# Kernel optimization log

Hardware: AMD Instinct MI355X
Metric: run time of the kernel (lower is better)

The kernel has to match this reference:

```python
import jax, jax.numpy as jnp
import numpy as np
from jax import lax

H = 20  # hidden_size


def _rnn_layer(x_seq, h0, W_ih, W_hh, b_ih, b_hh):
    """Vanilla tanh RNN layer. x_seq: [B,T,D], h0: [B,H]. Returns ([B,T,H], [B,H])."""
    # Precompute input projection for all timesteps (the only large GEMM).
    xp = jnp.einsum('btd,hd->bth', x_seq, W_ih) + b_ih + b_hh  # [B,T,H]

    def step(h, xt):
        h = jnp.tanh(xt + h @ W_hh.T)
        return h, h

    h_last, hs = lax.scan(step, h0, jnp.swapaxes(xp, 0, 1))  # hs: [T,B,H]
    return jnp.swapaxes(hs, 0, 1), h_last


def setup_inputs() -> dict:
    key = jax.random.key(0)
    ks = jax.random.split(key, 12)
    B, T = 4096, 512
    s = 1.0 / np.sqrt(H)  # PyTorch default uniform(-1/sqrt(H), 1/sqrt(H))
    u = lambda k, shape: jax.random.uniform(k, shape, jnp.float32, -s, s)
    return {
        'x': jax.random.normal(ks[0], (B, T, 1), jnp.float32),
        'hidden': jax.random.normal(ks[1], (2, B, H), jnp.float32),
        'W_ih0': u(ks[2], (H, 1)),
        'W_hh0': u(ks[3], (H, H)),
        'b_ih0': u(ks[4], (H,)),
        'b_hh0': u(ks[5], (H,)),
        'W_ih1': u(ks[6], (H, H)),
        'W_hh1': u(ks[7], (H, H)),
        'b_ih1': u(ks[8], (H,)),
        'b_hh1': u(ks[9], (H,)),
        'fc_w': u(ks[10], (1, H)),
        'fc_b': u(ks[11], (1,)),
    }


def reference(x, hidden, W_ih0, W_hh0, b_ih0, b_hh0, W_ih1, W_hh1, b_ih1, b_hh1, fc_w, fc_b):
    # 2-layer vanilla RNN (eval mode: inter-layer dropout disabled)
    h0_seq, h0_last = _rnn_layer(x, hidden[0], W_ih0, W_hh0, b_ih0, b_hh0)
    h1_seq, h1_last = _rnn_layer(h0_seq, hidden[1], W_ih1, W_hh1, b_ih1, b_hh1)
    out = h1_seq[:, -1, :] @ fc_w.T + fc_b  # [B,1]
    new_hidden = jnp.stack([h0_last, h1_last], axis=0)  # [2,B,H]
    return out, new_hidden
```

## Files before the change

### kernel.cpp

```cpp
#include <hip/hip_runtime.h>


#define Bsz 4096
#define Tn  512
#define Hn  20
#define GB  2
#define XPAD 520
#define NTHREADS 64

typedef float v2 __attribute__((ext_vector_type(2)));

__device__ __forceinline__ float tanh_fast(float v) {
    float e = __expf(2.0f * v);
    return 1.0f - 2.0f * __builtin_amdgcn_rcpf(e + 1.0f);
}

#define DOT20P(acc, accb, W, H) do { \
    acc  = __builtin_elementwise_fma(W##0, H##0, acc);  \
    accb = __builtin_elementwise_fma(W##1, H##1, accb); \
    acc  = __builtin_elementwise_fma(W##2, H##2, acc);  \
    accb = __builtin_elementwise_fma(W##3, H##3, accb); \
    acc  = __builtin_elementwise_fma(W##4, H##4, acc);  \
    accb = __builtin_elementwise_fma(W##5, H##5, accb); \
    acc  = __builtin_elementwise_fma(W##6, H##6, acc);  \
    accb = __builtin_elementwise_fma(W##7, H##7, accb); \
    acc  = __builtin_elementwise_fma(W##8, H##8, acc);  \
    accb = __builtin_elementwise_fma(W##9, H##9, accb); \
} while (0)

#define LOAD_ROWP(W, ptr) \
    v2 W##0, W##1, W##2, W##3, W##4, W##5, W##6, W##7, W##8, W##9; \
    { const float4* _p = (const float4*)(ptr); \
      float4 _t; \
      _t = _p[0]; W##0 = (v2){_t.x, _t.y}; W##1 = (v2){_t.z, _t.w}; \
      _t = _p[1]; W##2 = (v2){_t.x, _t.y}; W##3 = (v2){_t.z, _t.w}; \
      _t = _p[2]; W##4 = (v2){_t.x, _t.y}; W##5 = (v2){_t.z, _t.w}; \
      _t = _p[3]; W##6 = (v2){_t.x, _t.y}; W##7 = (v2){_t.z, _t.w}; \
      _t = _p[4]; W##8 = (v2){_t.x, _t.y}; W##9 = (v2){_t.z, _t.w}; }

#define READ_H(H, base) \
    v2 H##0, H##1, H##2, H##3, H##4, H##5, H##6, H##7, H##8, H##9; \
    { const float4 _a = *(const float4*)((base) + 0);  \
      const float4 _b = *(const float4*)((base) + 4);  \
      const float4 _c = *(const float4*)((base) + 8);  \
      const float4 _d = *(const float4*)((base) + 12); \
      const float4 _e = *(const float4*)((base) + 16); \
      H##0 = (v2){_a.x, _a.y}; H##1 = (v2){_a.z, _a.w}; \
      H##2 = (v2){_b.x, _b.y}; H##3 = (v2){_b.z, _b.w}; \
      H##4 = (v2){_c.x, _c.y}; H##5 = (v2){_c.z, _c.w}; \
      H##6 = (v2){_d.x, _d.y}; H##7 = (v2){_d.z, _d.w}; \
      H##8 = (v2){_e.x, _e.y}; H##9 = (v2){_e.z, _e.w}; }

__global__ __launch_bounds__(NTHREADS)
__attribute__((amdgpu_waves_per_eu(1, 2)))
void rnn2_fused(const float* __restrict__ x,
                const float* __restrict__ hidden,
                const float* __restrict__ W_ih0,
                const float* __restrict__ W_hh0,
                const float* __restrict__ b_ih0,
                const float* __restrict__ b_hh0,
                const float* __restrict__ W_ih1,
                const float* __restrict__ W_hh1,
                const float* __restrict__ b_ih1,
                const float* __restrict__ b_hh1,
                const float* __restrict__ fc_w,
                const float* __restrict__ fc_b,
                float* __restrict__ out)
{
    const int tid = threadIdx.x;
    int g = tid / Hn;
    int j = tid - g * Hn;
    if (g >= GB) { g = GB - 1; j = tid % Hn; }
    const int  b        = blockIdx.x * GB + g;
    const bool b_ok     = (b < Bsz);
    const int  bl       = b_ok ? b : (Bsz - 1);
    const bool store_ok = (tid < GB * Hn) && b_ok;

    __shared__ float xs[GB][XPAD];
    __shared__ float hs[2][GB][Hn];

    LOAD_ROWP(w0, W_hh0 + j * Hn)
    LOAD_ROWP(w1, W_ih1 + j * Hn)
    LOAD_ROWP(w2, W_hh1 + j * Hn)

    const float wih0  = W_ih0[j];
    const float bias0 = b_ih0[j] + b_hh0[j];
    const float bias1 = b_ih1[j] + b_hh1[j];

    {
        const int bB = blockIdx.x * GB;
        #pragma unroll
        for (int r = 0; r < (GB * Tn) / (NTHREADS * 4); ++r) {
            const int c  = (r * NTHREADS + tid) * 4;
            const int gg = c >> 9;
            const int t  = c & (Tn - 1);
            const int bb = (bB + gg < Bsz) ? (bB + gg) : (Bsz - 1);
            float4 v = *(const float4*)(x + (long)bb * Tn + t);
            *(float4*)&xs[gg][t] = v;
        }
    }

    hs[0][g][j] = hidden[bl * Hn + j];
    hs[1][g][j] = hidden[(long)Bsz * Hn + bl * Hn + j];

    {
        READ_H(hA, &hs[0][g][0])
        v2 a0  = (v2){fmaf(xs[g][0], wih0, bias0), 0.f};
        v2 a0b = (v2){0.f, 0.f};
        DOT20P(a0, a0b, w0, hA);
        v2 s0 = a0 + a0b;
        hs[0][g][j] = tanh_fast(s0.x + s0.y);
    }

    #pragma unroll 4
    for (int i = 1; i < Tn; ++i) {
        READ_H(hA, &hs[0][g][0])
        READ_H(hB, &hs[1][g][0])

        const float xt = xs[g][i];

        v2 a0  = (v2){fmaf(xt, wih0, bias0), 0.f};
        v2 a0b = (v2){0.f, 0.f};
        v2 a1  = (v2){bias1, 0.f};
        v2 a1b = (v2){0.f, 0.f};
        v2 a2  = (v2){0.f, 0.f};
        v2 a2b = (v2){0.f, 0.f};
        DOT20P(a0, a0b, w0, hA);
        DOT20P(a1, a1b, w1, hA);
        DOT20P(a2, a2b, w2, hB);

        const v2 s0 = a0 + a0b;
        const v2 s1 = (a1 + a1b) + (a2 + a2b);
        const float n0 = tanh_fast(s0.x + s0.y);
        const float n1 = tanh_fast(s1.x + s1.y);
        hs[0][g][j] = n0;
        hs[1][g][j] = n1;
    }

    {
        READ_H(hA, &hs[0][g][0])
        READ_H(hB, &hs[1][g][0])
        v2 a1  = (v2){bias1, 0.f};
        v2 a1b = (v2){0.f, 0.f};
        v2 a2  = (v2){0.f, 0.f};
        v2 a2b = (v2){0.f, 0.f};
        DOT20P(a1, a1b, w1, hA);
        DOT20P(a2, a2b, w2, hB);
        const v2 s1 = (a1 + a1b) + (a2 + a2b);
        hs[1][g][j] = tanh_fast(s1.x + s1.y);
    }

    if (store_ok) {
        out[Bsz + (long)b * Hn + j]                  = hs[0][g][j];
        out[Bsz + (long)Bsz * Hn + (long)b * Hn + j] = hs[1][g][j];
        if (j == 0) {
            LOAD_ROWP(fw, fc_w)
            READ_H(hv, &hs[1][g][0])
            v2 aA = (v2){fc_b[0], 0.f};
            v2 aB = (v2){0.f, 0.f};
            DOT20P(aA, aB, fw, hv);
            const v2 s = aA + aB;
            out[b] = s.x + s.y;
        }
    }
}

extern "C" void kernel_launch(void* const* d_in, const int* in_sizes, int n_in,
                              void* d_out, int out_size, void* d_ws, size_t ws_size,
                              hipStream_t stream) {
    const float* x      = (const float*)d_in[0];
    const float* hidden = (const float*)d_in[1];
    const float* W_ih0  = (const float*)d_in[2];
    const float* W_hh0  = (const float*)d_in[3];
    const float* b_ih0  = (const float*)d_in[4];
    const float* b_hh0  = (const float*)d_in[5];
    const float* W_ih1  = (const float*)d_in[6];
    const float* W_hh1  = (const float*)d_in[7];
    const float* b_ih1  = (const float*)d_in[8];
    const float* b_hh1  = (const float*)d_in[9];
    const float* fc_w   = (const float*)d_in[10];
    const float* fc_b   = (const float*)d_in[11];

    const int nblocks = (Bsz + GB - 1) / GB;
    rnn2_fused<<<nblocks, NTHREADS, 0, stream>>>(
        x, hidden, W_ih0, W_hh0, b_ih0, b_hh0,
        W_ih1, W_hh1, b_ih1, b_hh1, fc_w, fc_b, (float*)d_out);
}
```

Before: 134.6 us.

## Compute two hidden units per lane and pack four sequences per wave

Each lane now produces an even/odd pair of hidden units, so one 64-lane block holds 4 batch rows instead of 2. The grid halves, and each h vector read from LDS now feeds two dot products instead of one. The change also widens the hidden-state and output stores to float2 and tightens the occupancy hint to one wave per EU. In exchange, weight registers double (six 20-wide rows per lane) and the serial ALU chain per step is longer; the batch-bound guards are dropped on the assumption that Bsz divides by GB.

```diff
diff --git a/kernel.cpp b/kernel.cpp
--- a/kernel.cpp
+++ b/kernel.cpp
@@ -4,7 +4,8 @@
 #define Bsz 4096
 #define Tn  512
 #define Hn  20
-#define GB  2
+#define GB  4
+#define LPB 10
 #define XPAD 520
 #define NTHREADS 64
 
@@ -52,7 +53,7 @@
       H##8 = (v2){_e.x, _e.y}; H##9 = (v2){_e.z, _e.w}; }
 
 __global__ __launch_bounds__(NTHREADS)
-__attribute__((amdgpu_waves_per_eu(1, 2)))
+__attribute__((amdgpu_waves_per_eu(1, 1)))
 void rnn2_fused(const float* __restrict__ x,
                 const float* __restrict__ hidden,
                 const float* __restrict__ W_ih0,
@@ -68,24 +69,28 @@
                 float* __restrict__ out)
 {
     const int tid = threadIdx.x;
-    int g = tid / Hn;
-    int j = tid - g * Hn;
-    if (g >= GB) { g = GB - 1; j = tid % Hn; }
-    const int  b        = blockIdx.x * GB + g;
-    const bool b_ok     = (b < Bsz);
-    const int  bl       = b_ok ? b : (Bsz - 1);
-    const bool store_ok = (tid < GB * Hn) && b_ok;
+    const int jj  = tid % LPB;
+    int g = tid / LPB;
+    if (g >= GB) g = GB - 1;
+    const int j0 = 2 * jj;
+    const int b  = blockIdx.x * GB + g;
+    const bool store_ok = (tid < GB * LPB);
 
     __shared__ float xs[GB][XPAD];
     __shared__ float hs[2][GB][Hn];
 
-    LOAD_ROWP(w0, W_hh0 + j * Hn)
-    LOAD_ROWP(w1, W_ih1 + j * Hn)
-    LOAD_ROWP(w2, W_hh1 + j * Hn)
-
-    const float wih0  = W_ih0[j];
-    const float bias0 = b_ih0[j] + b_hh0[j];
-    const float bias1 = b_ih1[j] + b_hh1[j];
+    LOAD_ROWP(w0e, W_hh0 + j0 * Hn)
+    LOAD_ROWP(w0o, W_hh0 + (j0 + 1) * Hn)
+    LOAD_ROWP(w1e, W_ih1 + j0 * Hn)
+    LOAD_ROWP(w1o, W_ih1 + (j0 + 1) * Hn)
+    LOAD_ROWP(w2e, W_hh1 + j0 * Hn)
+    LOAD_ROWP(w2o, W_hh1 + (j0 + 1) * Hn)
+
+    const float wih0e = W_ih0[j0],  wih0o = W_ih0[j0 + 1];
+    const float b0e = b_ih0[j0]     + b_hh0[j0];
+    const float b0o = b_ih0[j0 + 1] + b_hh0[j0 + 1];
+    const float b1e = b_ih1[j0]     + b_hh1[j0];
+    const float b1o = b_ih1[j0 + 1] + b_hh1[j0 + 1];
 
     {
         const int bB = blockIdx.x * GB;
@@ -94,22 +99,28 @@
             const int c  = (r * NTHREADS + tid) * 4;
             const int gg = c >> 9;
             const int t  = c & (Tn - 1);
-            const int bb = (bB + gg < Bsz) ? (bB + gg) : (Bsz - 1);
-            float4 v = *(const float4*)(x + (long)bb * Tn + t);
+            float4 v = *(const float4*)(x + (long)(bB + gg) * Tn + t);
             *(float4*)&xs[gg][t] = v;
         }
     }
 
-    hs[0][g][j] = hidden[bl * Hn + j];
-    hs[1][g][j] = hidden[(long)Bsz * Hn + bl * Hn + j];
+    {
+        float2 h0i = *(const float2*)(hidden + b * Hn + j0);
+        float2 h1i = *(const float2*)(hidden + (long)Bsz * Hn + b * Hn + j0);
+        *(float2*)&hs[0][g][j0] = h0i;
+        *(float2*)&hs[1][g][j0] = h1i;
+    }
 
     {
         READ_H(hA, &hs[0][g][0])
-        v2 a0  = (v2){fmaf(xs[g][0], wih0, bias0), 0.f};
-        v2 a0b = (v2){0.f, 0.f};
-        DOT20P(a0, a0b, w0, hA);
-        v2 s0 = a0 + a0b;
-        hs[0][g][j] = tanh_fast(s0.x + s0.y);
+        const float xt = xs[g][0];
+        v2 a0e = (v2){fmaf(xt, wih0e, b0e), 0.f}, a0eb = (v2){0.f, 0.f};
+        v2 a0o = (v2){fmaf(xt, wih0o, b0o), 0.f}, a0ob = (v2){0.f, 0.f};
+        DOT20P(a0e, a0eb, w0e, hA);
+        DOT20P(a0o, a0ob, w0o, hA);
+        const v2 se = a0e + a0eb, so = a0o + a0ob;
+        *(float2*)&hs[0][g][j0] =
+            make_float2(tanh_fast(se.x + se.y), tanh_fast(so.x + so.y));
     }
 
     #pragma unroll 4
@@ -119,41 +130,52 @@
 
         const float xt = xs[g][i];
 
-        v2 a0  = (v2){fmaf(xt, wih0, bias0), 0.f};
-        v2 a0b = (v2){0.f, 0.f};
-        v2 a1  = (v2){bias1, 0.f};
-        v2 a1b = (v2){0.f, 0.f};
-        v2 a2  = (v2){0.f, 0.f};
-        v2 a2b = (v2){0.f, 0.f};
-        DOT20P(a0, a0b, w0, hA);
-        DOT20P(a1, a1b, w1, hA);
-        DOT20P(a2, a2b, w2, hB);
-
-        const v2 s0 = a0 + a0b;
-        const v2 s1 = (a1 + a1b) + (a2 + a2b);
-        const float n0 = tanh_fast(s0.x + s0.y);
-        const float n1 = tanh_fast(s1.x + s1.y);
-        hs[0][g][j] = n0;
-        hs[1][g][j] = n1;
+        v2 a0e = (v2){fmaf(xt, wih0e, b0e), 0.f}, a0eb = (v2){0.f, 0.f};
+        v2 a0o = (v2){fmaf(xt, wih0o, b0o), 0.f}, a0ob = (v2){0.f, 0.f};
+        v2 a1e = (v2){b1e, 0.f}, a1eb = (v2){0.f, 0.f};
+        v2 a1o = (v2){b1o, 0.f}, a1ob = (v2){0.f, 0.f};
+        v2 a2e = (v2){0.f, 0.f}, a2eb = (v2){0.f, 0.f};
+        v2 a2o = (v2){0.f, 0.f}, a2ob = (v2){0.f, 0.f};
+
+        DOT20P(a0e, a0eb, w0e, hA);
+        DOT20P(a0o, a0ob, w0o, hA);
+        DOT20P(a1e, a1eb, w1e, hA);
+        DOT20P(a1o, a1ob, w1o, hA);
+        DOT20P(a2e, a2eb, w2e, hB);
+        DOT20P(a2o, a2ob, w2o, hB);
+
+        const v2 s0e = a0e + a0eb, s0o = a0o + a0ob;
+        const v2 s1e = (a1e + a1eb) + (a2e + a2eb);
+        const v2 s1o = (a1o + a1ob) + (a2o + a2ob);
+        *(float2*)&hs[0][g][j0] =
+            make_float2(tanh_fast(s0e.x + s0e.y), tanh_fast(s0o.x + s0o.y));
+        *(float2*)&hs[1][g][j0] =
+            make_float2(tanh_fast(s1e.x + s1e.y), tanh_fast(s1o.x + s1o.y));
     }
 
     {
         READ_H(hA, &hs[0][g][0])
         READ_H(hB, &hs[1][g][0])
-        v2 a1  = (v2){bias1, 0.f};
-        v2 a1b = (v2){0.f, 0.f};
-        v2 a2  = (v2){0.f, 0.f};
-        v2 a2b = (v2){0.f, 0.f};
-        DOT20P(a1, a1b, w1, hA);
-        DOT20P(a2, a2b, w2, hB);
-        const v2 s1 = (a1 + a1b) + (a2 + a2b);
-        hs[1][g][j] = tanh_fast(s1.x + s1.y);
+        v2 a1e = (v2){b1e, 0.f}, a1eb = (v2){0.f, 0.f};
+        v2 a1o = (v2){b1o, 0.f}, a1ob = (v2){0.f, 0.f};
+        v2 a2e = (v2){0.f, 0.f}, a2eb = (v2){0.f, 0.f};
+        v2 a2o = (v2){0.f, 0.f}, a2ob = (v2){0.f, 0.f};
+        DOT20P(a1e, a1eb, w1e, hA);
+        DOT20P(a1o, a1ob, w1o, hA);
+        DOT20P(a2e, a2eb, w2e, hB);
+        DOT20P(a2o, a2ob, w2o, hB);
+        const v2 s1e = (a1e + a1eb) + (a2e + a2eb);
+        const v2 s1o = (a1o + a1ob) + (a2o + a2ob);
+        *(float2*)&hs[1][g][j0] =
+            make_float2(tanh_fast(s1e.x + s1e.y), tanh_fast(s1o.x + s1o.y));
     }
 
     if (store_ok) {
-        out[Bsz + (long)b * Hn + j]                  = hs[0][g][j];
-        out[Bsz + (long)Bsz * Hn + (long)b * Hn + j] = hs[1][g][j];
-        if (j == 0) {
+        *(float2*)(out + Bsz + (long)b * Hn + j0) =
+            *(const float2*)&hs[0][g][j0];
+        *(float2*)(out + Bsz + (long)Bsz * Hn + (long)b * Hn + j0) =
+            *(const float2*)&hs[1][g][j0];
+        if (jj == 0) {
             LOAD_ROWP(fw, fc_w)
             READ_H(hv, &hs[1][g][0])
             v2 aA = (v2){fc_b[0], 0.f};
@@ -181,7 +203,7 @@
     const float* fc_w   = (const float*)d_in[10];
     const float* fc_b   = (const float*)d_in[11];
 
-    const int nblocks = (Bsz + GB - 1) / GB;
+    const int nblocks = Bsz / GB;
     rnn2_fused<<<nblocks, NTHREADS, 0, stream>>>(
         x, hidden, W_ih0, W_hh0, b_ih0, b_hh0,
         W_ih1, W_hh1, b_ih1, b_hh1, fc_w, fc_b, (float*)d_out);
```

After: 139.0 us. 1.03x slower.
